# Performance work log

Hardware: AMD Instinct MI355X
Metric: run time of the kernel (lower is better)

The kernel has to match this reference:

```python
import jax, jax.numpy as jnp
import numpy as np

LEAK = 0.2
EPS_LN = 1e-5   # nn.LayerNorm default
EPS_IN = 1e-5   # nn.InstanceNorm2d default
EPS_D = 1e-8    # demodulation eps


def _leaky(x):
    return jnp.where(x >= 0, x, LEAK * x)


def _layernorm(s, g, b):
    mu = s.mean(-1, keepdims=True)
    v = ((s - mu) ** 2).mean(-1, keepdims=True)
    return (s - mu) / jnp.sqrt(v + EPS_LN) * g + b


def _instnorm(x):
    # per (b, c) normalization over HW, no affine (InstanceNorm2d default)
    mu = x.mean((2, 3), keepdims=True)
    v = ((x - mu) ** 2).mean((2, 3), keepdims=True)
    return (x - mu) / jnp.sqrt(v + EPS_IN)


def _conv(x, wt, pad):
    # x: [B,C,H,W], wt: [O,I,k,k]
    return jax.lax.conv_general_dilated(
        x, wt, (1, 1), [(pad, pad), (pad, pad)],
        dimension_numbers=('NCHW', 'OIHW', 'NCHW'))


def _modconv(x, w, wt, scale, mw, mb, lg, lb, asw, asb, abw, abb, demod):
    # style -> per-sample per-in-channel modulation
    s = _leaky(_layernorm(w @ mw.T + mb, lg, lb))              # [b, in]
    wb = wt[None] * (s[:, None, :, None, None] * scale[None])  # [b, O, I, k, k]
    # AdaIN on the input (use_adain=True in this block)
    sc = (w @ asw.T + asb)[:, :, None, None]
    bi = (w @ abw.T + abb)[:, :, None, None]
    x = sc * _instnorm(x) + bi
    if demod:
        d = jax.lax.rsqrt(jnp.sum(wb * wb, axis=(2, 3, 4)) + EPS_D)  # [b, O]
        wb = wb * d[:, :, None, None, None]
    pad = wt.shape[-1] // 2
    # per-sample conv == groups=b grouped conv in the torch original
    return jax.vmap(lambda xi, wi: _conv(xi[None], wi, pad)[0])(x, wb)


def _upsample2x(x):
    B, C, H, W = x.shape
    # bilinear, half-pixel centers == torch align_corners=False
    return jax.image.resize(x, (B, C, 2 * H, 2 * W), 'bilinear')


def setup_inputs() -> dict:
    key = jax.random.key(0)
    ks = iter(jax.random.split(key, 64))
    B, Cin, Cout, L, H = 8, 128, 64, 512, 128
    rn = lambda shape, s=1.0: jax.random.normal(next(ks), shape, jnp.float32) * s
    lin = 1.0 / float(np.sqrt(L))
    return dict(
        x=rn((B, Cin, H, H)), w=rn((B, L)),
        w1=rn((Cout, Cin, 3, 3), 0.02), sc1=jnp.ones((1, Cin, 1, 1), jnp.float32),
        m1_w=rn((Cin, L), lin), m1_b=jnp.zeros((Cin,), jnp.float32),
        ln1_g=jnp.ones((Cin,), jnp.float32), ln1_b=jnp.zeros((Cin,), jnp.float32),
        a1_sw=rn((Cin, L), lin), a1_sb=jnp.zeros((Cin,), jnp.float32),
        a1_bw=rn((Cin, L), lin), a1_bb=jnp.zeros((Cin,), jnp.float32),
        w25=rn((4, Cout, Cout, 3, 3), 0.02), sc25=jnp.ones((4, 1, Cout, 1, 1), jnp.float32),
        m25_w=rn((4, Cout, L), lin), m25_b=jnp.zeros((4, Cout), jnp.float32),
        ln25_g=jnp.ones((4, Cout), jnp.float32), ln25_b=jnp.zeros((4, Cout), jnp.float32),
        a25_sw=rn((4, Cout, L), lin), a25_sb=jnp.zeros((4, Cout), jnp.float32),
        a25_bw=rn((4, Cout, L), lin), a25_bb=jnp.zeros((4, Cout), jnp.float32),
        wr=rn((3, Cout, 1, 1), 0.02), scr=jnp.ones((1, Cout, 1, 1), jnp.float32),
        mr_w=rn((Cout, L), lin), mr_b=jnp.zeros((Cout,), jnp.float32),
        lnr_g=jnp.ones((Cout,), jnp.float32), lnr_b=jnp.zeros((Cout,), jnp.float32),
        ar_sw=rn((Cout, L), lin), ar_sb=jnp.zeros((Cout,), jnp.float32),
        ar_bw=rn((Cout, L), lin), ar_bb=jnp.zeros((Cout,), jnp.float32),
        sk_w=rn((Cout, Cin, 1, 1), 0.02), sk_b=jnp.zeros((Cout,), jnp.float32),
    )


def reference(x, w, w1, sc1, m1_w, m1_b, ln1_g, ln1_b, a1_sw, a1_sb, a1_bw, a1_bb,
              w25, sc25, m25_w, m25_b, ln25_g, ln25_b, a25_sw, a25_sb, a25_bw, a25_bb,
              wr, scr, mr_w, mr_b, lnr_g, lnr_b, ar_sw, ar_sb, ar_bw, ar_bb,
              sk_w, sk_b):
    x = _upsample2x(x)
    skip = _conv(x, sk_w, 0) + sk_b[None, :, None, None]
    h = _leaky(_modconv(x, w, w1, sc1, m1_w, m1_b, ln1_g, ln1_b,
                        a1_sw, a1_sb, a1_bw, a1_bb, True))
    for i in range(4):  # conv2..conv5, identical structure
        h = _leaky(_modconv(h, w, w25[i], sc25[i], m25_w[i], m25_b[i],
                            ln25_g[i], ln25_b[i], a25_sw[i], a25_sb[i],
                            a25_bw[i], a25_bb[i], True))
    h = h + skip
    rgb = _modconv(h, w, wr, scr, mr_w, mr_b, lnr_g, lnr_b,
                   ar_sw, ar_sb, ar_bw, ar_bb, False)
    return h, rgb
```

## Files before the change

kernel.cpp:

```cpp
#include <hip/hip_runtime.h>
#include <cstdint>

#define LEAK 0.2f

typedef __attribute__((ext_vector_type(8))) short bf16x8;
typedef __attribute__((ext_vector_type(4))) float f32x4;

__device__ __forceinline__ float leaky(float v){ return v >= 0.f ? v : LEAK*v; }

__device__ __forceinline__ uint32_t f32_to_bf16_rne(float v){
    uint32_t u = __float_as_uint(v);
    return (u + 0x7fffu + ((u >> 16) & 1u)) >> 16;
}
__device__ __forceinline__ uint32_t split_pack(float v){
    uint32_t u = __float_as_uint(v);
    uint32_t hb = (u + 0x7fffu + ((u >> 16) & 1u)) & 0xffff0000u;
    float lof = v - __uint_as_float(hb);
    uint32_t lo = f32_to_bf16_rne(lof);
    return (hb >> 16) | (lo << 16);
}

__global__ __launch_bounds__(128)
void style_kernel(const float* __restrict__ w,
                  const float* __restrict__ mw, const float* __restrict__ mb,
                  const float* __restrict__ lng, const float* __restrict__ lnb,
                  const float* __restrict__ asw, const float* __restrict__ asb,
                  const float* __restrict__ abw, const float* __restrict__ abb,
                  const float* __restrict__ sc, int Cin,
                  float* __restrict__ out_sm, float* __restrict__ out_asc,
                  float* __restrict__ out_abi)
{
    __shared__ float wl[512];
    __shared__ float red[128];
    int b = blockIdx.x;
    int tid = threadIdx.x;
    for (int j = tid; j < 512; j += 128) wl[j] = w[b*512 + j];
    __syncthreads();

    float t = 0.f, ascv = 0.f, abiv = 0.f;
    if (tid < Cin) {
        const float* r1 = mw  + (size_t)tid*512;
        const float* r2 = asw + (size_t)tid*512;
        const float* r3 = abw + (size_t)tid*512;
        for (int j = 0; j < 512; ++j) {
            float wj = wl[j];
            t    = fmaf(wj, r1[j], t);
            ascv = fmaf(wj, r2[j], ascv);
            abiv = fmaf(wj, r3[j], abiv);
        }
        t += mb[tid]; ascv += asb[tid]; abiv += abb[tid];
    }
    red[tid] = (tid < Cin) ? t : 0.f;
    __syncthreads();
    for (int s = 64; s > 0; s >>= 1) { if (tid < s) red[tid] += red[tid+s]; __syncthreads(); }
    float mu = red[0] / (float)Cin;
    __syncthreads();
    float dv = (tid < Cin) ? (t - mu) : 0.f;
    red[tid] = dv*dv;
    __syncthreads();
    for (int s = 64; s > 0; s >>= 1) { if (tid < s) red[tid] += red[tid+s]; __syncthreads(); }
    float var = red[0] / (float)Cin;
    float rstd = rsqrtf(var + 1e-5f);
    if (tid < Cin) {
        float sln = (t - mu) * rstd * lng[tid] + lnb[tid];
        sln = leaky(sln);
        out_sm[b*128 + tid]  = sln * sc[tid];
        out_asc[b*128 + tid] = ascv;
        out_abi[b*128 + tid] = abiv;
    }
}

__global__ __launch_bounds__(128)
void demod_kernel(const float* __restrict__ w1, const float* __restrict__ w25,
                  const float* __restrict__ sty, float* __restrict__ dout)
{
    int bid = blockIdx.x;
    int o = bid & 63;
    int b = (bid >> 6) & 7;
    int l = bid >> 9;
    int Cin = (l == 0) ? 128 : 64;
    const float* wt = (l == 0) ? (w1 + (size_t)o*128*9)
                               : (w25 + ((size_t)(l-1)*64 + o)*64*9);
    const float* smL = sty + l*3072 + b*128;
    int tid = threadIdx.x;
    float sum = 0.f;
    for (int i = tid; i < Cin; i += 128) {
        float s = smL[i];
        const float* wp = wt + i*9;
        float acc = 0.f;
        #pragma unroll
        for (int k = 0; k < 9; ++k) { float ww = wp[k]; acc = fmaf(ww, ww, acc); }
        sum = fmaf(acc, s*s, sum);
    }
    __shared__ float red[128];
    red[tid] = sum; __syncthreads();
    for (int s = 64; s > 0; s >>= 1) { if (tid < s) red[tid] += red[tid+s]; __syncthreads(); }
    if (tid == 0) dout[l*512 + b*64 + o] = rsqrtf(red[0] + 1e-8f);
}

__global__ __launch_bounds__(256)
void upsample_pack_kernel(const float* __restrict__ x, uint32_t* __restrict__ Up,
                          float* __restrict__ sums)
{
    int bid = blockIdx.x;
    int b = bid >> 8, y = bid & 255;
    int tid = threadIdx.x;
    int c = tid & 15, pg = tid >> 4;
    int q = y >> 1; int rlo, rhi; float wlo, whi;
    if (y & 1) { rlo = q; rhi = (q+1 < 127) ? q+1 : 127; wlo = 0.75f; whi = 0.25f; }
    else       { rlo = (q-1 > 0) ? q-1 : 0; rhi = q;     wlo = 0.25f; whi = 0.75f; }
    __shared__ float xs[2][16][129];
    __shared__ float red2[2][4][16];
    for (int cg = 0; cg < 8; ++cg) {
        __syncthreads();
        for (int e = tid; e < 4096; e += 256) {
            int row = e >> 11, cc = (e >> 7) & 15, px = e & 127;
            xs[row][cc][px] = x[((size_t)(b*128 + cg*16 + cc) << 14) + (row ? rhi : rlo)*128 + px];
        }
        __syncthreads();
        float s = 0.f, sq = 0.f;
        uint32_t* base = Up + ((((size_t)(b*8 + cg)*256 + y)*256))*16 + c;
        #pragma unroll
        for (int k = 0; k < 16; ++k) {
            int px = pg*16 + k;
            int m = px >> 1;
            float v;
            if (px & 1) {
                int m2 = (m+1 < 127) ? m+1 : 127;
                float vc = wlo*xs[0][c][m]  + whi*xs[1][c][m];
                float vr = wlo*xs[0][c][m2] + whi*xs[1][c][m2];
                v = 0.75f*vc + 0.25f*vr;
            } else {
                int m0 = (m-1 > 0) ? m-1 : 0;
                float vl = wlo*xs[0][c][m0] + whi*xs[1][c][m0];
                float vc = wlo*xs[0][c][m]  + whi*xs[1][c][m];
                v = 0.25f*vl + 0.75f*vc;
            }
            s += v; sq += v*v;
            base[(size_t)px*16] = split_pack(v);
        }
        s  += __shfl_xor(s, 16);  s  += __shfl_xor(s, 32);
        sq += __shfl_xor(sq, 16); sq += __shfl_xor(sq, 32);
        int wid = tid >> 6;
        if ((tid & 63) < 16) { red2[0][wid][c] = s; red2[1][wid][c] = sq; }
        __syncthreads();
        if (tid < 16) {
            float S = red2[0][0][tid] + red2[0][1][tid] + red2[0][2][tid] + red2[0][3][tid];
            float Q = red2[1][0][tid] + red2[1][1][tid] + red2[1][2][tid] + red2[1][3][tid];
            atomicAdd(&sums[(b*128 + cg*16 + tid)*2],     S);
            atomicAdd(&sums[(b*128 + cg*16 + tid)*2 + 1], Q);
        }
    }
}

__global__ __launch_bounds__(256)
void packskip_kernel(const float* __restrict__ skw, uint16_t* __restrict__ skp)
{
    int e = blockIdx.x*256 + threadIdx.x;
    if (e >= 8192) return;
    int o = e >> 7, i = e & 127;
    uint32_t pk = split_pack(skw[e]);
    int ic = i >> 4, cl = i & 15, cg = cl >> 2, j2 = (cl & 3)*2;
    uint16_t* dst = skp + ic*2048 + (o >> 4)*512 + cg*128 + (o & 15)*8 + j2;
    dst[0] = (uint16_t)(pk & 0xffffu);
    dst[1] = (uint16_t)(pk >> 16);
}

template<int CIN>
__global__ __launch_bounds__(CIN)
void packw_kernel(const float* __restrict__ wt, const float* __restrict__ sty,
                  const float* __restrict__ sums,
                  uint16_t* __restrict__ wp, float* __restrict__ bias9)
{
    int b = blockIdx.x >> 6;
    int o = blockIdx.x & 63;
    int i = threadIdx.x;

    float sm = sty[b*128 + i];
    float av = sty[1024 + b*128 + i];
    float bv = sty[2048 + b*128 + i];
    float s0 = sums[(b*CIN + i)*2], s1 = sums[(b*CIN + i)*2 + 1];
    float m = s0 * (1.f/65536.f);
    float var = s1 * (1.f/65536.f) - m*m;
    float r = rsqrtf((var > 0.f ? var : 0.f) + 1e-5f);
    float A  = sm * av * r;
    float Bv = sm * (bv - av*m*r);

    const float* wrow = wt + ((size_t)o*CIN + i)*9;
    float c9[9];
    #pragma unroll
    for (int k = 0; k < 9; ++k) c9[k] = wrow[k];

    const int NCH = CIN/16;
    int ic = i >> 4, cl = i & 15, cg = cl >> 2, j2 = (cl & 3)*2;
    uint16_t* wpb = wp + ((size_t)b*NCH + ic)*18432;
    #pragma unroll
    for (int k = 0; k < 9; ++k) {
        float wv = c9[k] * A;
        uint32_t pk = split_pack(wv);
        uint16_t* dst = wpb + k*2048 + (o >> 4)*512 + cg*128 + (o & 15)*8 + j2;
        dst[0] = (uint16_t)(pk & 0xffffu);
        dst[1] = (uint16_t)(pk >> 16);
    }

    float colS[3][3];
    #pragma unroll
    for (int ky = 0; ky < 3; ++ky) {
        colS[ky][0] = c9[ky*3+1] + c9[ky*3+2];
        colS[ky][1] = c9[ky*3+0] + c9[ky*3+1] + c9[ky*3+2];
        colS[ky][2] = c9[ky*3+0] + c9[ky*3+1];
    }
    float part[9];
    #pragma unroll
    for (int rx = 0; rx < 3; ++rx) {
        part[0*3+rx] = colS[1][rx] + colS[2][rx];
        part[1*3+rx] = colS[0][rx] + colS[1][rx] + colS[2][rx];
        part[2*3+rx] = colS[0][rx] + colS[1][rx];
    }
    __shared__ float red[9][CIN];
    #pragma unroll
    for (int t = 0; t < 9; ++t) red[t][i] = part[t] * Bv;
    __syncthreads();
    for (int s = CIN/2; s > 0; s >>= 1) {
        if (i < s) {
            #pragma unroll
            for (int t = 0; t < 9; ++t) red[t][i] += red[t][i + s];
        }
        __syncthreads();
    }
    if (i < 9) bias9[((size_t)(b*64 + o))*9 + i] = red[i][0];
}

template<int CIN, int MODE, bool SKIP>
__global__ __launch_bounds__(512)
void conv_mfma_kernel(const uint32_t* __restrict__ inPair,
                      const uint16_t* __restrict__ Wp,
                      const float* __restrict__ bias9,
                      const float* __restrict__ dmod,
                      const uint16_t* __restrict__ skp,
                      const float* __restrict__ skb,
                      float* __restrict__ skipOut,
                      uint32_t* __restrict__ outPair,
                      float* __restrict__ outF32,
                      float* __restrict__ statsH)
{
    __shared__ __align__(16) unsigned char LDS[78464];
    const int tid = threadIdx.x;
    const int lane = tid & 63, wv = tid >> 6;
    const int rw = wv >> 2, oq = wv & 3;

    int bid = blockIdx.x;
    bid = (bid & 7) * 256 + (bid >> 3);
    const int xh = bid & 1, yb = (bid >> 1) & 127, b = bid >> 8;
    const int y0 = yb*2, x0 = xh*128;

    union U8 { uint32_t u[4]; bf16x8 v; };

    f32x4 acc[8];
    f32x4 accS[SKIP ? 8 : 1];
    #pragma unroll
    for (int q = 0; q < 8; ++q) acc[q] = (f32x4){0.f, 0.f, 0.f, 0.f};
    if constexpr (SKIP) {
        #pragma unroll
        for (int q = 0; q < 8; ++q) accS[q] = (f32x4){0.f, 0.f, 0.f, 0.f};
    }

    const int NCH = CIN/16;
    for (int ic = 0; ic < NCH; ++ic) {
        uint4 sfrag;
        if constexpr (SKIP)
            sfrag = *reinterpret_cast<const uint4*>(
                skp + ic*2048 + oq*512 + (lane >> 4)*128 + (lane & 15)*8);
        {
            const uint16_t* wsrc = Wp + ((size_t)b*NCH + ic)*18432;
            for (int e = tid; e < 2304; e += 512) {
                uint4 v = *reinterpret_cast<const uint4*>(wsrc + e*8);
                *reinterpret_cast<uint4*>(LDS + 41600 + e*16) = v;
            }
        }
        for (int e = tid; e < 2080; e += 512) {
            int part = e & 3;
            int pr = e >> 2;
            int px = pr % 130, row = pr / 130;
            int yy = y0 - 1 + row, xx = x0 - 1 + px;
            uint4 v = {0u, 0u, 0u, 0u};
            if (yy >= 0 && yy < 256 && xx >= 0 && xx < 256)
                v = *reinterpret_cast<const uint4*>(
                    inPair + ((((size_t)b*NCH + ic)*256 + yy)*256 + xx)*16 + part*4);
            *reinterpret_cast<uint4*>(LDS + row*10400 + px*80 + part*16) = v;
        }
        __syncthreads();
        #pragma unroll
        for (int tap = 0; tap < 9; ++tap) {
            const int dy1 = tap/3, dxm = tap % 3;
            uint4 wv4 = *reinterpret_cast<const uint4*>(
                LDS + 41600 + tap*4096 + oq*1024 + (lane >> 4)*256 + (lane & 15)*16);
            U8 wa, wb;
            #pragma unroll
            for (int q = 0; q < 4; ++q) {
                uint32_t ww = (&wv4.x)[q];
                wa.u[q] = __builtin_amdgcn_perm(ww, ww, 0x01000100u);
                wb.u[q] = __builtin_amdgcn_perm(ww, ww, 0x03020302u);
            }
            U8 sa, sb;
            if constexpr (SKIP) {
                if (tap == 4) {
                    #pragma unroll
                    for (int q = 0; q < 4; ++q) {
                        uint32_t ww = (&sfrag.x)[q];
                        sa.u[q] = __builtin_amdgcn_perm(ww, ww, 0x01000100u);
                        sb.u[q] = __builtin_amdgcn_perm(ww, ww, 0x03020302u);
                    }
                }
            }
            const int rowbase = (rw + dy1)*10400 + (lane >> 4)*16 + ((lane & 15) + dxm)*80;
            #pragma unroll
            for (int xf = 0; xf < 8; ++xf) {
                bf16x8 bf = *reinterpret_cast<const bf16x8*>(LDS + rowbase + xf*1280);
                acc[xf] = __builtin_amdgcn_mfma_f32_16x16x32_bf16(wa.v, bf, acc[xf], 0, 0, 0);
                acc[xf] = __builtin_amdgcn_mfma_f32_16x16x32_bf16(wb.v, bf, acc[xf], 0, 0, 0);
                if constexpr (SKIP) {
                    if (tap == 4) {
                        accS[xf] = __builtin_amdgcn_mfma_f32_16x16x32_bf16(sa.v, bf, accS[xf], 0, 0, 0);
                        accS[xf] = __builtin_amdgcn_mfma_f32_16x16x32_bf16(sb.v, bf, accS[xf], 0, 0, 0);
                    }
                }
            }
        }
        __syncthreads();
    }

    const int y = y0 + rw;
    const int ry = (y == 0) ? 0 : ((y == 255) ? 2 : 1);
    float dv4[4], bmid[4], bl[4], br[4], skb4[4];
    #pragma unroll
    for (int r2 = 0; r2 < 4; ++r2) {
        int o = oq*16 + (lane >> 4)*4 + r2;
        dv4[r2] = dmod[b*64 + o];
        const float* bp = bias9 + ((size_t)(b*64 + o))*9 + ry*3;
        bmid[r2] = bp[1];
        bl[r2] = bmid[r2]; br[r2] = bmid[r2];
        if (x0 == 0   && (lane & 15) == 0)  bl[r2] = bp[0];
        if (x0 == 128 && (lane & 15) == 15) br[r2] = bp[2];
        if constexpr (SKIP) skb4[r2] = skb[o];
    }

    float s4[4] = {0.f,0.f,0.f,0.f}, q4[4] = {0.f,0.f,0.f,0.f};
    #pragma unroll
    for (int xf = 0; xf < 8; ++xf) {
        #pragma unroll
        for (int r2 = 0; r2 < 4; ++r2) {
            float bias = (xf == 0) ? bl[r2] : ((xf == 7) ? br[r2] : bmid[r2]);
            float v = (acc[xf][r2] + bias) * dv4[r2];
            v = leaky(v);
            acc[xf][r2] = v;
            if (MODE != 2) { s4[r2] += v; q4[r2] += v*v; }
        }
    }

    if constexpr (SKIP) {
        #pragma unroll
        for (int xf = 0; xf < 8; ++xf) {
            #pragma unroll
            for (int r2 = 0; r2 < 4; ++r2) {
                int o = oq*16 + (lane >> 4)*4 + r2;
                size_t addr = ((size_t)(b*64 + o))*65536 + (size_t)y*256 + x0 + xf*16 + (lane & 15);
                skipOut[addr] = accS[xf][r2] + skb4[r2];
            }
        }
    }

    if constexpr (MODE == 2) {
        #pragma unroll
        for (int xf = 0; xf < 8; ++xf) {
            #pragma unroll
            for (int r2 = 0; r2 < 4; ++r2) {
                int o = oq*16 + (lane >> 4)*4 + r2;
                size_t addr = ((size_t)(b*64 + o))*65536 + (size_t)y*256 + x0 + xf*16 + (lane & 15);
                float v = acc[xf][r2] + outF32[addr];
                outF32[addr] = v;
                s4[r2] += v; q4[r2] += v*v;
            }
        }
    }

    #pragma unroll
    for (int r2 = 0; r2 < 4; ++r2) {
        #pragma unroll
        for (int w = 1; w < 16; w <<= 1) {
            s4[r2] += __shfl_xor(s4[r2], w);
            q4[r2] += __shfl_xor(q4[r2], w);
        }
    }
    if ((lane & 15) == 0) {
        #pragma unroll
        for (int r2 = 0; r2 < 4; ++r2) {
            int o = oq*16 + (lane >> 4)*4 + r2;
            atomicAdd(&statsH[(b*64 + o)*2],     s4[r2]);
            atomicAdd(&statsH[(b*64 + o)*2 + 1], q4[r2]);
        }
    }

    if constexpr (MODE != 2) {
        uint32_t* outb = outPair + ((((size_t)b*4 + oq)*256 + y)*256 + x0)*16 + (lane >> 4)*4;
        #pragma unroll
        for (int xf = 0; xf < 8; ++xf) {
            int px = xf*16 + (lane & 15);
            uint4 pk4;
            pk4.x = split_pack(acc[xf][0]);
            pk4.y = split_pack(acc[xf][1]);
            pk4.z = split_pack(acc[xf][2]);
            pk4.w = split_pack(acc[xf][3]);
            *reinterpret_cast<uint4*>(outb + (size_t)px*16) = pk4;
        }
    }
}

__global__ __launch_bounds__(256)
void rgb_kernel(const float* __restrict__ h, const float* __restrict__ wr,
                const float* __restrict__ sty, const float* __restrict__ sums,
                float* __restrict__ rgb)
{
    __shared__ float A[64], Bc[64];
    __shared__ float wl[192];
    int bid = blockIdx.x;
    int b = bid >> 7;
    int px0 = (bid & 127) * 512;
    int tid = threadIdx.x;
    if (tid < 64) {
        float smv = sty[b*128 + tid];
        float av  = sty[1024 + b*128 + tid];
        float bv  = sty[2048 + b*128 + tid];
        float s0 = sums[(b*64 + tid)*2], s1 = sums[(b*64 + tid)*2 + 1];
        float m = s0 * (1.f/65536.f);
        float var = s1 * (1.f/65536.f) - m*m;
        float r = rsqrtf((var > 0.f ? var : 0.f) + 1e-5f);
        A[tid]  = smv * av * r;
        Bc[tid] = smv * (bv - av*m*r);
    }
    if (tid < 192) wl[tid] = wr[tid];
    __syncthreads();
    int pix = px0 + tid*2;
    const float* hp = h + (size_t)b*64*65536 + pix;
    float a0[3] = {0,0,0}, a1[3] = {0,0,0};
    for (int i = 0; i < 64; ++i) {
        float2 v = *reinterpret_cast<const float2*>(hp + (size_t)i*65536);
        float xi0 = fmaf(A[i], v.x, Bc[i]);
        float xi1 = fmaf(A[i], v.y, Bc[i]);
        #pragma unroll
        for (int o = 0; o < 3; ++o) {
            float wv = wl[o*64 + i];
            a0[o] = fmaf(wv, xi0, a0[o]);
            a1[o] = fmaf(wv, xi1, a1[o]);
        }
    }
    float* rp = rgb + (size_t)b*3*65536 + pix;
    #pragma unroll
    for (int o = 0; o < 3; ++o)
        *reinterpret_cast<float2*>(rp + (size_t)o*65536) = make_float2(a0[o], a1[o]);
}

extern "C" void kernel_launch(void* const* d_in, const int* in_sizes, int n_in,
                              void* d_out, int out_size, void* d_ws, size_t ws_size,
                              hipStream_t stream)
{
    const float* x     = (const float*)d_in[0];
    const float* w     = (const float*)d_in[1];
    const float* w1    = (const float*)d_in[2];
    const float* sc1   = (const float*)d_in[3];
    const float* m1_w  = (const float*)d_in[4];
    const float* m1_b  = (const float*)d_in[5];
    const float* ln1_g = (const float*)d_in[6];
    const float* ln1_b = (const float*)d_in[7];
    const float* a1_sw = (const float*)d_in[8];
    const float* a1_sb = (const float*)d_in[9];
    const float* a1_bw = (const float*)d_in[10];
    const float* a1_bb = (const float*)d_in[11];
    const float* w25   = (const float*)d_in[12];
    const float* sc25  = (const float*)d_in[13];
    const float* m25_w = (const float*)d_in[14];
    const float* m25_b = (const float*)d_in[15];
    const float* ln25_g= (const float*)d_in[16];
    const float* ln25_b= (const float*)d_in[17];
    const float* a25_sw= (const float*)d_in[18];
    const float* a25_sb= (const float*)d_in[19];
    const float* a25_bw= (const float*)d_in[20];
    const float* a25_bb= (const float*)d_in[21];
    const float* wr    = (const float*)d_in[22];
    const float* scr   = (const float*)d_in[23];
    const float* mr_w  = (const float*)d_in[24];
    const float* mr_b  = (const float*)d_in[25];
    const float* lnr_g = (const float*)d_in[26];
    const float* lnr_b = (const float*)d_in[27];
    const float* ar_sw = (const float*)d_in[28];
    const float* ar_sb = (const float*)d_in[29];
    const float* ar_bw = (const float*)d_in[30];
    const float* ar_bb = (const float*)d_in[31];
    const float* sk_w  = (const float*)d_in[32];
    const float* sk_b  = (const float*)d_in[33];

    float* outp    = (float*)d_out;
    float* h_out   = outp;
    float* rgb_out = outp + (size_t)33554432;

    uint8_t* ws = (uint8_t*)d_ws;
    uint32_t*  Upair  = (uint32_t*)(ws + 0);
    uint32_t*  hpB    = (uint32_t*)(ws + 0);
    uint32_t*  hpA    = (uint32_t*)(ws + 268435456ull);
    uint16_t*  WpBase = (uint16_t*)(ws + 402653184ull);
    float*     sty    = (float*)(ws + 409731072ull);
    float*     dmod   = (float*)(ws + 409804800ull);
    float*     stats  = (float*)(ws + 409815040ull);
    float*     bias9  = (float*)(ws + 409843712ull);
    uint16_t*  skp    = (uint16_t*)(ws + 409935872ull);

    float* sumsU = stats;
    float* st1   = stats + 2048;
    float* st2   = stats + 3072;
    float* st3   = stats + 4096;
    float* st4   = stats + 5120;
    float* st5   = stats + 6144;

    uint16_t* Wp1 = WpBase;
    uint16_t* Wp2 = WpBase + 1179648;
    uint16_t* Wp3 = Wp2 + 589824;
    uint16_t* Wp4 = Wp3 + 589824;
    uint16_t* Wp5 = Wp4 + 589824;

    hipMemsetAsync(stats, 0, 28672, stream);

    style_kernel<<<8,128,0,stream>>>(w, m1_w, m1_b, ln1_g, ln1_b, a1_sw, a1_sb,
                                     a1_bw, a1_bb, sc1, 128,
                                     sty, sty+1024, sty+2048);
    for (int l = 1; l <= 4; ++l) {
        int j = l - 1;
        style_kernel<<<8,128,0,stream>>>(w, m25_w + (size_t)j*32768, m25_b + j*64,
                                         ln25_g + j*64, ln25_b + j*64,
                                         a25_sw + (size_t)j*32768, a25_sb + j*64,
                                         a25_bw + (size_t)j*32768, a25_bb + j*64,
                                         sc25 + j*64, 64,
                                         sty + l*3072, sty + l*3072 + 1024, sty + l*3072 + 2048);
    }
    style_kernel<<<8,128,0,stream>>>(w, mr_w, mr_b, lnr_g, lnr_b, ar_sw, ar_sb,
                                     ar_bw, ar_bb, scr, 64,
                                     sty + 5*3072, sty + 5*3072 + 1024, sty + 5*3072 + 2048);

    demod_kernel<<<2560,128,0,stream>>>(w1, w25, sty, dmod);
    packskip_kernel<<<32,256,0,stream>>>(sk_w, skp);

    upsample_pack_kernel<<<2048,256,0,stream>>>(x, Upair, sumsU);

    packw_kernel<128><<<512,128,0,stream>>>(w1, sty, sumsU, Wp1, bias9);
    conv_mfma_kernel<128,1,true><<<2048,512,0,stream>>>(Upair, Wp1, bias9, dmod,
                                                        skp, sk_b, h_out,
                                                        hpA, nullptr, st1);
    packw_kernel<64><<<512,64,0,stream>>>(w25, sty + 3072, st1, Wp2, bias9 + 4608);
    conv_mfma_kernel<64,1,false><<<2048,512,0,stream>>>(hpA, Wp2, bias9 + 4608, dmod + 512,
                                                        nullptr, nullptr, nullptr,
                                                        hpB, nullptr, st2);
    packw_kernel<64><<<512,64,0,stream>>>(w25 + 36864, sty + 2*3072, st2, Wp3, bias9 + 2*4608);
    conv_mfma_kernel<64,1,false><<<2048,512,0,stream>>>(hpB, Wp3, bias9 + 2*4608, dmod + 2*512,
                                                        nullptr, nullptr, nullptr,
                                                        hpA, nullptr, st3);
    packw_kernel<64><<<512,64,0,stream>>>(w25 + 2*36864, sty + 3*3072, st3, Wp4, bias9 + 3*4608);
    conv_mfma_kernel<64,1,false><<<2048,512,0,stream>>>(hpA, Wp4, bias9 + 3*4608, dmod + 3*512,
                                                        nullptr, nullptr, nullptr,
                                                        hpB, nullptr, st4);
    packw_kernel<64><<<512,64,0,stream>>>(w25 + 3*36864, sty + 4*3072, st4, Wp5, bias9 + 4*4608);
    conv_mfma_kernel<64,2,false><<<2048,512,0,stream>>>(hpB, Wp5, bias9 + 4*4608, dmod + 4*512,
                                                        nullptr, nullptr, nullptr,
                                                        nullptr, h_out, st5);

    rgb_kernel<<<1024,256,0,stream>>>(h_out, wr, sty + 5*3072, st5, rgb_out);
}
```

Before: 1.479 ms.

## Prefetch next input chunk into registers during MFMA compute in 64-channel convs

For the four 64-input-channel conv layers, the loop over input-channel chunks becomes a register-prefetch pipeline. The next chunk's input halo is loaded into registers while the current chunk's MFMAs run from LDS, and wave priority is raised around the compute. The goal is to hide global-memory latency behind the matrix math without adding LDS. The cost is extra VGPRs, which could cause spills or lower occupancy at 512 threads per block. The first conv keeps the original path.

```diff
diff --git a/kernel.cpp b/kernel.cpp
--- a/kernel.cpp
+++ b/kernel.cpp
@@ -231,7 +231,7 @@
     if (i < 9) bias9[((size_t)(b*64 + o))*9 + i] = red[i][0];
 }
 
-template<int CIN, int MODE, bool SKIP>
+template<int CIN, int MODE, bool SKIP, int PIPE>
 __global__ __launch_bounds__(512)
 void conv_mfma_kernel(const uint32_t* __restrict__ inPair,
                       const uint16_t* __restrict__ Wp,
@@ -266,30 +266,15 @@
     }
 
     const int NCH = CIN/16;
-    for (int ic = 0; ic < NCH; ++ic) {
-        uint4 sfrag;
-        if constexpr (SKIP)
-            sfrag = *reinterpret_cast<const uint4*>(
-                skp + ic*2048 + oq*512 + (lane >> 4)*128 + (lane & 15)*8);
-        {
-            const uint16_t* wsrc = Wp + ((size_t)b*NCH + ic)*18432;
-            for (int e = tid; e < 2304; e += 512) {
-                uint4 v = *reinterpret_cast<const uint4*>(wsrc + e*8);
-                *reinterpret_cast<uint4*>(LDS + 41600 + e*16) = v;
-            }
-        }
-        for (int e = tid; e < 2080; e += 512) {
-            int part = e & 3;
-            int pr = e >> 2;
-            int px = pr % 130, row = pr / 130;
-            int yy = y0 - 1 + row, xx = x0 - 1 + px;
-            uint4 v = {0u, 0u, 0u, 0u};
-            if (yy >= 0 && yy < 256 && xx >= 0 && xx < 256)
-                v = *reinterpret_cast<const uint4*>(
-                    inPair + ((((size_t)b*NCH + ic)*256 + yy)*256 + xx)*16 + part*4);
-            *reinterpret_cast<uint4*>(LDS + row*10400 + px*80 + part*16) = v;
-        }
-        __syncthreads();
+
+    auto stageW = [&](int ic) {
+        const uint16_t* wsrc = Wp + ((size_t)b*NCH + ic)*18432;
+        for (int e = tid; e < 2304; e += 512) {
+            uint4 v = *reinterpret_cast<const uint4*>(wsrc + e*8);
+            *reinterpret_cast<uint4*>(LDS + 41600 + e*16) = v;
+        }
+    };
+    auto computeChunk = [&](int ic) {
         #pragma unroll
         for (int tap = 0; tap < 9; ++tap) {
             const int dy1 = tap/3, dxm = tap % 3;
@@ -305,6 +290,8 @@
             U8 sa, sb;
             if constexpr (SKIP) {
                 if (tap == 4) {
+                    uint4 sfrag = *reinterpret_cast<const uint4*>(
+                        skp + ic*2048 + oq*512 + (lane >> 4)*128 + (lane & 15)*8);
                     #pragma unroll
                     for (int q = 0; q < 4; ++q) {
                         uint32_t ww = (&sfrag.x)[q];
@@ -327,7 +314,66 @@
                 }
             }
         }
-        __syncthreads();
+    };
+
+    if constexpr (PIPE == 0) {
+        for (int ic = 0; ic < NCH; ++ic) {
+            stageW(ic);
+            for (int e = tid; e < 2080; e += 512) {
+                int part = e & 3;
+                int pr = e >> 2;
+                int px = pr % 130, row = pr / 130;
+                int yy = y0 - 1 + row, xx = x0 - 1 + px;
+                uint4 v = {0u, 0u, 0u, 0u};
+                if (yy >= 0 && yy < 256 && xx >= 0 && xx < 256)
+                    v = *reinterpret_cast<const uint4*>(
+                        inPair + ((((size_t)b*NCH + ic)*256 + yy)*256 + xx)*16 + part*4);
+                *reinterpret_cast<uint4*>(LDS + row*10400 + px*80 + part*16) = v;
+            }
+            __syncthreads();
+            computeChunk(ic);
+            __syncthreads();
+        }
+    } else {
+        uint4 xr[5];
+        auto loadX = [&](int ic) {
+            #pragma unroll
+            for (int k = 0; k < 5; ++k) {
+                if (k < 4 || tid < 32) {
+                    int e = tid + k*512;
+                    int part = e & 3;
+                    int pr = e >> 2;
+                    int px = pr % 130, row = pr / 130;
+                    int yy = y0 - 1 + row, xx = x0 - 1 + px;
+                    uint4 v = {0u, 0u, 0u, 0u};
+                    if (yy >= 0 && yy < 256 && xx >= 0 && xx < 256)
+                        v = *reinterpret_cast<const uint4*>(
+                            inPair + ((((size_t)b*NCH + ic)*256 + yy)*256 + xx)*16 + part*4);
+                    xr[k] = v;
+                }
+            }
+        };
+        loadX(0);
+        #pragma unroll
+        for (int ic = 0; ic < 4; ++ic) {
+            stageW(ic);
+            #pragma unroll
+            for (int k = 0; k < 5; ++k) {
+                if (k < 4 || tid < 32) {
+                    int e = tid + k*512;
+                    int part = e & 3;
+                    int pr = e >> 2;
+                    int px = pr % 130, row = pr / 130;
+                    *reinterpret_cast<uint4*>(LDS + row*10400 + px*80 + part*16) = xr[k];
+                }
+            }
+            __syncthreads();
+            if (ic + 1 < 4) loadX(ic + 1);
+            __builtin_amdgcn_s_setprio(1);
+            computeChunk(ic);
+            __builtin_amdgcn_s_setprio(0);
+            __syncthreads();
+        }
     }
 
     const int y = y0 + rw;
@@ -551,25 +597,25 @@
     upsample_pack_kernel<<<2048,256,0,stream>>>(x, Upair, sumsU);
 
     packw_kernel<128><<<512,128,0,stream>>>(w1, sty, sumsU, Wp1, bias9);
-    conv_mfma_kernel<128,1,true><<<2048,512,0,stream>>>(Upair, Wp1, bias9, dmod,
-                                                        skp, sk_b, h_out,
-                                                        hpA, nullptr, st1);
+    conv_mfma_kernel<128,1,true,0><<<2048,512,0,stream>>>(Upair, Wp1, bias9, dmod,
+                                                          skp, sk_b, h_out,
+                                                          hpA, nullptr, st1);
     packw_kernel<64><<<512,64,0,stream>>>(w25, sty + 3072, st1, Wp2, bias9 + 4608);
-    conv_mfma_kernel<64,1,false><<<2048,512,0,stream>>>(hpA, Wp2, bias9 + 4608, dmod + 512,
-                                                        nullptr, nullptr, nullptr,
-                                                        hpB, nullptr, st2);
+    conv_mfma_kernel<64,1,false,1><<<2048,512,0,stream>>>(hpA, Wp2, bias9 + 4608, dmod + 512,
+                                                          nullptr, nullptr, nullptr,
+                                                          hpB, nullptr, st2);
     packw_kernel<64><<<512,64,0,stream>>>(w25 + 36864, sty + 2*3072, st2, Wp3, bias9 + 2*4608);
-    conv_mfma_kernel<64,1,false><<<2048,512,0,stream>>>(hpB, Wp3, bias9 + 2*4608, dmod + 2*512,
-                                                        nullptr, nullptr, nullptr,
-                                                        hpA, nullptr, st3);
+    conv_mfma_kernel<64,1,false,1><<<2048,512,0,stream>>>(hpB, Wp3, bias9 + 2*4608, dmod + 2*512,
+                                                          nullptr, nullptr, nullptr,
+                                                          hpA, nullptr, st3);
     packw_kernel<64><<<512,64,0,stream>>>(w25 + 2*36864, sty + 3*3072, st3, Wp4, bias9 + 3*4608);
-    conv_mfma_kernel<64,1,false><<<2048,512,0,stream>>>(hpA, Wp4, bias9 + 3*4608, dmod + 3*512,
-                                                        nullptr, nullptr, nullptr,
-                                                        hpB, nullptr, st4);
+    conv_mfma_kernel<64,1,false,1><<<2048,512,0,stream>>>(hpA, Wp4, bias9 + 3*4608, dmod + 3*512,
+                                                          nullptr, nullptr, nullptr,
+                                                          hpB, nullptr, st4);
     packw_kernel<64><<<512,64,0,stream>>>(w25 + 3*36864, sty + 4*3072, st4, Wp5, bias9 + 4*4608);
-    conv_mfma_kernel<64,2,false><<<2048,512,0,stream>>>(hpB, Wp5, bias9 + 4*4608, dmod + 4*512,
-                                                        nullptr, nullptr, nullptr,
-                                                        nullptr, h_out, st5);
+    conv_mfma_kernel<64,2,false,1><<<2048,512,0,stream>>>(hpB, Wp5, bias9 + 4*4608, dmod + 4*512,
+                                                          nullptr, nullptr, nullptr,
+                                                          nullptr, h_out, st5);
 
     rgb_kernel<<<1024,256,0,stream>>>(h_out, wr, sty + 5*3072, st5, rgb_out);
 }
```

Result: slower. 1.694 ms (+14.5%).
